# Kernel tuning notes

Measured on AMD Instinct MI355X. Metric: run time of the kernel, lower is better.

## Reference

```python
import jax, jax.numpy as jnp
import numpy as np

B, V, K = 4, 16384, 16
E, F, D, H, L, ITERS = 32, 2, 64, 4, 2, 10
NEG = -1e9


def setup_inputs() -> dict:
    key = jax.random.key(0)
    ks = jax.random.split(key, 24)
    def g(k, shape, fan_in):
        return jax.random.normal(k, shape, dtype=jnp.float32) * (fan_in ** -0.5)
    inp = {}
    inp["node_embeddings"] = jax.random.normal(ks[0], (B, V, E), dtype=jnp.float32)
    inp["node_features"] = jax.random.normal(ks[1], (B, V, F), dtype=jnp.float32)
    inp["demands"] = jax.random.normal(ks[2], (B, V, 1), dtype=jnp.float32)
    # padded adjacency list; value == V means masked (no neighbor)
    inp["adj_lst"] = jax.random.randint(ks[3], (B, V, K), 0, V + 1, dtype=jnp.int32)
    # precomputed inverse-adjacency indices; reference computes inflow by scatter-add instead
    inp["flow_indices"] = jax.random.randint(ks[4], (B, V, K), 0, V, dtype=jnp.int32)
    inp["num_nodes"] = V
    din = E + F
    inp["W_enc1"] = g(ks[5], (din, D), din); inp["b_enc1"] = jnp.zeros((D,), jnp.float32)
    inp["W_enc2"] = g(ks[6], (D, D), D); inp["b_enc2"] = jnp.zeros((D,), jnp.float32)
    inp["W_gat"] = g(ks[7], (H, D, D), D)
    inp["a_src"] = g(ks[8], (H, D), D)
    inp["a_dst"] = g(ks[9], (H, D), D)
    for i, nm in enumerate(["z", "r", "c"]):
        inp["W_" + nm] = g(ks[10 + 2 * i], (D, D), D)
        inp["U_" + nm] = g(ks[11 + 2 * i], (D, D), D)
        inp["b_" + nm] = jnp.zeros((D,), jnp.float32)
    inp["W_dec1"] = g(ks[16], (D, D), D); inp["b_dec1"] = jnp.zeros((D,), jnp.float32)
    inp["W_dec2"] = g(ks[17], (D, 1), D); inp["b_dec2"] = jnp.zeros((1,), jnp.float32)
    return inp


def _forward(node_embeddings, node_features, demands,
             W_enc1, b_enc1, W_enc2, b_enc2,
             W_gat, a_src, a_dst,
             W_z, U_z, b_z, W_r, U_r, b_r, W_c, U_c, b_c,
             W_dec1, b_dec1, W_dec2, b_dec2,
             adj_lst, num_nodes):
    Vn = num_nodes
    bidx = jnp.arange(adj_lst.shape[0])[:, None, None]  # [B,1,1]
    mask = adj_lst == Vn  # [B,V,K] padded slots

    # --- node encoder MLP (tanh, activate_final=True) ---
    x = jnp.concatenate([node_embeddings, node_features], axis=-1)
    h = jnp.tanh(x @ W_enc1 + b_enc1)
    h = jnp.tanh(h @ W_enc2 + b_enc2)

    def gather_nodes(t):
        # masked_gather: pad with a zero row so index == num_nodes reads zeros
        t_pad = jnp.concatenate([t, jnp.zeros_like(t[:, :1])], axis=1)  # [B,V+1,Dt]
        return t_pad[bidx, adj_lst]  # [B,V,K,Dt]

    # --- graph_layers x (AdjGAT + GRU) ---
    for _ in range(L):
        agg = 0.0
        for hd in range(H):
            t = h @ W_gat[hd]                       # [B,V,D]
            nb = gather_nodes(t)                    # [B,V,K,D]
            scores = (t @ a_src[hd])[:, :, None] + nb @ a_dst[hd]  # [B,V,K]
            attn = jax.nn.softmax(jnp.where(mask, NEG, scores), axis=-1)
            agg = agg + jnp.einsum('bvk,bvkd->bvd', attn, nb)
        m = jnp.tanh(agg / H)
        z = jax.nn.sigmoid(m @ W_z + h @ U_z + b_z)
        r = jax.nn.sigmoid(m @ W_r + h @ U_r + b_r)
        c = jnp.tanh(m @ W_c + (r * h) @ U_c + b_c)
        h = (1.0 - z) * h + z * c

    # --- decoder -> per-edge weights via masked gather + softmax ---
    node_w = jnp.tanh(h @ W_dec1 + b_dec1) @ W_dec2 + b_dec2   # [B,V,1]
    pw = gather_nodes(node_w)[..., 0]                          # [B,V,K]
    norm_w = jax.nn.softmax(jnp.where(mask, NEG, pw), axis=-1)

    # --- iterative min-cost-flow solver ---
    flow0 = norm_w * jax.nn.relu(-demands)  # sources (demand<0) push supply
    def body(carry, _):
        flow, _ = carry
        inflow = jnp.zeros((flow.shape[0], Vn + 1), flow.dtype)
        inflow = inflow.at[bidx, adj_lst].add(flow)[:, :Vn]    # [B,V]
        new = norm_w * jax.nn.relu(inflow[..., None] - demands)
        return (new, flow), None
    (flow, pflow), _ = jax.lax.scan(body, (flow0, flow0), None, length=ITERS)

    flow_cost = jnp.sum(flow * flow, axis=(1, 2))  # quadratic cost_fn
    return flow, flow_cost, norm_w, pflow


def reference(node_embeddings, node_features, demands, adj_lst, flow_indices, num_nodes,
              W_enc1, b_enc1, W_enc2, b_enc2, W_gat, a_src, a_dst,
              W_z, U_z, b_z, W_r, U_r, b_r, W_c, U_c, b_c,
              W_dec1, b_dec1, W_dec2, b_dec2):
    # flow_indices is the precomputed inverse adjacency; inflow is computed
    # equivalently here by scatter-add over adj_lst.
    return _forward(node_embeddings, node_features, demands,
                    W_enc1, b_enc1, W_enc2, b_enc2,
                    W_gat, a_src, a_dst,
                    W_z, U_z, b_z, W_r, U_r, b_r, W_c, U_c, b_c,
                    W_dec1, b_dec1, W_dec2, b_dec2,
                    adj_lst, num_nodes)
```

## Files before the change

### kernel.cpp

```cpp
#include <hip/hip_runtime.h>
#include <stdint.h>
#include <math.h>

#define BN 4
#define VN 16384
#define KN 16
#define HN 4
#define NN (BN*VN)
#define EN (VN*KN)
#define CAP 64
#define NEGC (-1.0e9f)

typedef __attribute__((ext_vector_type(8))) short short8;
typedef __attribute__((ext_vector_type(4))) float floatx4;
typedef __attribute__((ext_vector_type(2))) float floatx2;
typedef unsigned short u16;
typedef unsigned int u32;

#define OFF_H      0ull
#define OFF_T      16777216ull
#define OFF_M      50331648ull
#define OFF_SSRC   67108864ull
#define OFF_SDST   68157440ull
#define OFF_NW     69206016ull
#define OFF_NV     69468160ull
#define OFF_CNT    69992448ull
#define OFF_PG     70254848ull
#define OFF_PZR    (OFF_PG  + 32768ull)
#define OFF_PC     (OFF_PZR + 32768ull)
#define OFF_PE1    (OFF_PC  + 16384ull)
#define OFF_PE2    (OFF_PE1 + 8192ull)
#define OFF_PD1    (OFF_PE2 + 8192ull)

__device__ __forceinline__ u16 f2bf(float x){
  union { float f; unsigned int u; } c; c.f = x;
  unsigned int r = c.u + 0x7fffu + ((c.u >> 16) & 1u);
  return (u16)(r >> 16);
}
__device__ __forceinline__ float bf2f(u16 s){
  union { unsigned int u; float f; } c; c.u = ((unsigned int)s) << 16;
  return c.f;
}
__device__ __forceinline__ float sigm(float x){ return 1.0f/(1.0f+expf(-x)); }

union S8 { short8 v; u16 u[8]; };
union FU { float f; u32 u; };

__global__ __launch_bounds__(256) void k_zero(u32* __restrict__ cnt)
{
  cnt[blockIdx.x*256 + threadIdx.x] = 0u;
}

__global__ __launch_bounds__(256) void k_pack(
    const float* __restrict__ Wg,  const float* __restrict__ Wz, const float* __restrict__ Uz,
    const float* __restrict__ Wr,  const float* __restrict__ Ur, const float* __restrict__ Wc,
    const float* __restrict__ Uc,  const float* __restrict__ We1, const float* __restrict__ We2,
    const float* __restrict__ Wd1,
    u16* __restrict__ pg, u16* __restrict__ pzr, u16* __restrict__ pc,
    u16* __restrict__ pe1, u16* __restrict__ pe2, u16* __restrict__ pd1)
{
  int e = blockIdx.x*256 + threadIdx.x;
  int el; u16* dst; int CN; int region;
  if      (e < 16384){ el = e;        dst = pg;  CN = 2; region = 0; }
  else if (e < 32768){ el = e-16384;  dst = pzr; CN = 4; region = 1; }
  else if (e < 40960){ el = e-32768;  dst = pc;  CN = 4; region = 2; }
  else if (e < 45056){ el = e-40960;  dst = pe1; CN = 2; region = 3; }
  else if (e < 49152){ el = e-45056;  dst = pe2; CN = 2; region = 4; }
  else               { el = e-49152;  dst = pd1; CN = 2; region = 5; }
  int j    = el & 7;
  int lane = (el >> 3) & 63;
  int rest = el >> 9;
  int c  = rest % CN;
  int ng = rest / CN;
  int k  = c*32 + (lane>>4)*8 + j;
  int n  = ng*16 + (lane&15);
  float val = 0.0f;
  if (region == 0){
    val = Wg[(size_t)(n>>6)*4096 + k*64 + (n&63)];
  } else if (region == 1){
    int km = (k&3)*16 + ((k>>2)&15);
    if (n < 64) val = (k<64) ? Wz[km*64+n]      : Uz[(k-64)*64+n];
    else        val = (k<64) ? Wr[km*64+(n-64)] : Ur[(k-64)*64+(n-64)];
  } else if (region == 2){
    int km = (k&3)*16 + ((k>>2)&15);
    val = (k<64) ? Wc[km*64+n] : Uc[(k-64)*64+n];
  } else if (region == 3){
    val = (k<34) ? We1[k*64+n] : 0.0f;
  } else if (region == 4){
    val = We2[k*64+n];
  } else {
    val = Wd1[k*64+n];
  }
  dst[el] = f2bf(val);
}

template<int CN>
__device__ __forceinline__ void load_b(const u16* p, int chunk, int lane, short8 Bf[CN][4]){
  const short8* P = (const short8*)p;
  #pragma unroll
  for (int c=0;c<CN;c++)
    #pragma unroll
    for (int ng=0; ng<4; ng++)
      Bf[c][ng] = P[((chunk*4+ng)*CN + c)*64 + lane];
}

template<int CN>
__device__ __forceinline__ void mfma_tile(const short8* A, const short8 Bf[CN][4],
                                          floatx4 acc[4][4], int wave, int lane){
  #pragma unroll
  for (int c=0;c<CN;c++){
    #pragma unroll
    for (int mg=0;mg<4;mg++){
      short8 a = A[((wave*4+mg)*CN + c)*64 + lane];
      #pragma unroll
      for (int ng=0;ng<4;ng++)
        acc[mg][ng] = __builtin_amdgcn_mfma_f32_16x16x32_bf16(a, Bf[c][ng], acc[mg][ng], 0, 0, 0);
    }
  }
}

__device__ __forceinline__ void zero_acc(floatx4 acc[4][4]){
  #pragma unroll
  for (int mg=0;mg<4;mg++)
    #pragma unroll
    for (int ng=0;ng<4;ng++){
      floatx4 z = {0.f,0.f,0.f,0.f};
      acc[mg][ng] = z;
    }
}

__global__ __launch_bounds__(128) void k_enc(
    const float* __restrict__ emb, const float* __restrict__ feat,
    const u16* __restrict__ pe1, const u16* __restrict__ pe2,
    const float* __restrict__ be1, const float* __restrict__ be2,
    float* __restrict__ hout)
{
  __shared__ short8 A1[1024];
  __shared__ short8 A2[1024];
  const int tid = threadIdx.x;
  const int n0  = blockIdx.x * 128;
  for (int it=0; it<8; ++it){
    int slot = it*128 + tid;
    int row = slot >> 3, jc = slot & 7;
    S8 w;
    if (jc < 4){
      const float* s = emb + (size_t)(n0+row)*32 + jc*8;
      #pragma unroll
      for (int j=0;j<8;j++) w.u[j] = f2bf(s[j]);
    } else if (jc == 4){
      const float* s = feat + (size_t)(n0+row)*2;
      w.u[0] = f2bf(s[0]); w.u[1] = f2bf(s[1]);
      #pragma unroll
      for (int j=2;j<8;j++) w.u[j] = 0;
    } else {
      #pragma unroll
      for (int j=0;j<8;j++) w.u[j] = 0;
    }
    A1[((row>>4)*2 + (jc>>2))*64 + (jc&3)*16 + (row&15)] = w.v;
  }
  __syncthreads();
  const int wave = tid>>6, lane = tid&63, q = lane>>4, ml = lane&15;

  short8 Bf[2][4];
  load_b<2>(pe1, 0, lane, Bf);
  floatx4 acc[4][4];
  zero_acc(acc);
  mfma_tile<2>(A1, Bf, acc, wave, lane);

  u16* A2s = (u16*)A2;
  #pragma unroll
  for (int mg=0;mg<4;mg++){
    #pragma unroll
    for (int r=0;r<4;r++){
      int row_l = wave*64 + mg*16 + q*4 + r;
      #pragma unroll
      for (int ng=0;ng<4;ng++){
        int k2 = ng*16 + ml;
        float v = tanhf(acc[mg][ng][r] + be1[k2]);
        int c2 = k2>>5, q2=(k2>>3)&3, j2=k2&7;
        A2s[ (((row_l>>4)*2 + c2)*64 + q2*16 + (row_l&15))*8 + j2 ] = f2bf(v);
      }
    }
  }
  __syncthreads();

  load_b<2>(pe2, 0, lane, Bf);
  zero_acc(acc);
  mfma_tile<2>(A2, Bf, acc, wave, lane);
  #pragma unroll
  for (int mg=0;mg<4;mg++)
    #pragma unroll
    for (int r=0;r<4;r++){
      int row = n0 + wave*64 + mg*16 + q*4 + r;
      #pragma unroll
      for (int ng=0;ng<4;ng++){
        int col = ng*16 + ml;
        hout[(size_t)row*64 + col] = tanhf(acc[mg][ng][r] + be2[col]);
      }
    }
}

__global__ __launch_bounds__(128) void k_t(
    const float* __restrict__ h, const u16* __restrict__ pg,
    const float* __restrict__ asrc, const float* __restrict__ adst,
    u32* __restrict__ tq, float* __restrict__ ssrc, float* __restrict__ sdst)
{
  __shared__ short8 A[1024];
  const int tid = threadIdx.x;
  const int n0  = blockIdx.x * 128;
  for (int it=0; it<8; ++it){
    int slot = it*128 + tid;
    int row = slot >> 3, jc = slot & 7;
    const float* s = h + (size_t)(n0+row)*64 + jc*8;
    S8 w;
    #pragma unroll
    for (int j=0;j<8;j++) w.u[j] = f2bf(s[j]);
    A[((row>>4)*2 + (jc>>2))*64 + (jc&3)*16 + (row&15)] = w.v;
  }
  __syncthreads();
  const int wave = tid>>6, lane = tid&63, q = lane>>4, ml = lane&15;

  for (int chunk=0; chunk<4; ++chunk){
    short8 Bf[2][4];
    load_b<2>(pg, chunk, lane, Bf);
    floatx4 acc[4][4];
    zero_acc(acc);
    mfma_tile<2>(A, Bf, acc, wave, lane);

    float as[4], ad[4];
    #pragma unroll
    for (int ng=0;ng<4;ng++){
      as[ng] = asrc[chunk*64 + ng*16 + ml];
      ad[ng] = adst[chunk*64 + ng*16 + ml];
    }
    #pragma unroll
    for (int mg=0;mg<4;mg++){
      #pragma unroll
      for (int r=0;r<4;r++){
        int row = n0 + wave*64 + mg*16 + q*4 + r;
        float v0 = acc[mg][0][r], v1 = acc[mg][1][r];
        float v2 = acc[mg][2][r], v3 = acc[mg][3][r];
        int pk = __builtin_amdgcn_cvt_pk_fp8_f32(v0, v1, 0, false);
        pk     = __builtin_amdgcn_cvt_pk_fp8_f32(v2, v3, pk, true);
        tq[(size_t)row*64 + chunk*16 + ml] = (u32)pk;
        float ps = v0*as[0] + v1*as[1] + v2*as[2] + v3*as[3];
        float pd = v0*ad[0] + v1*ad[1] + v2*ad[2] + v3*ad[3];
        #pragma unroll
        for (int s=1;s<16;s<<=1){ ps += __shfl_xor(ps, s, 64); pd += __shfl_xor(pd, s, 64); }
        if (ml == 0){ ssrc[row*4 + chunk] = ps; sdst[row*4 + chunk] = pd; }
      }
    }
  }
}

__global__ __launch_bounds__(256) void k_attn(
    const int* __restrict__ adj, const u32* __restrict__ tq,
    const float* __restrict__ ssrc, const float* __restrict__ sdst,
    float* __restrict__ m)
{
  const int wave = threadIdx.x>>6, lane = threadIdx.x&63;
  const int nid = blockIdx.x*4 + wave;
  const int b = nid >> 14;
  const int hd = lane>>4;
  int u = adj[(size_t)nid*16 + (lane&15)];
  float sc = (u == VN) ? NEGC : (ssrc[nid*4 + hd] + sdst[((size_t)b*VN + u)*4 + hd]);
  float mx = sc;
  #pragma unroll
  for (int s=1;s<16;s<<=1) mx = fmaxf(mx, __shfl_xor(mx, s, 64));
  float ex = expf(sc - mx);
  float sm = ex;
  #pragma unroll
  for (int s=1;s<16;s<<=1) sm += __shfl_xor(sm, s, 64);
  float attn = ex / sm;

  float a0=0.f, a1=0.f, a2=0.f, a3=0.f;
  const int srcl = lane & 48;
  #pragma unroll
  for (int k2=0;k2<16;k2++){
    int u2 = __shfl(u, k2, 64);
    float av = __shfl(attn, srcl + k2, 64);
    u32 w = tq[((size_t)b*VN + u2)*64 + lane];
    floatx2 f01 = __builtin_amdgcn_cvt_pk_f32_fp8((int)w, false);
    floatx2 f23 = __builtin_amdgcn_cvt_pk_f32_fp8((int)w, true);
    a0 += av*f01.x; a1 += av*f01.y; a2 += av*f23.x; a3 += av*f23.y;
  }
  a0 += __shfl_xor(a0,16,64); a0 += __shfl_xor(a0,32,64);
  a1 += __shfl_xor(a1,16,64); a1 += __shfl_xor(a1,32,64);
  a2 += __shfl_xor(a2,16,64); a2 += __shfl_xor(a2,32,64);
  a3 += __shfl_xor(a3,16,64); a3 += __shfl_xor(a3,32,64);
  if (lane < 16){
    floatx4 val;
    val[0] = tanhf(a0*0.25f); val[1] = tanhf(a1*0.25f);
    val[2] = tanhf(a2*0.25f); val[3] = tanhf(a3*0.25f);
    *(floatx4*)(m + (size_t)nid*64 + lane*4) = val;
  }
}

__global__ __launch_bounds__(128) void k_gru(
    const float* __restrict__ m, float* __restrict__ h,
    const u16* __restrict__ pzr, const u16* __restrict__ pc_,
    const float* __restrict__ bz, const float* __restrict__ br,
    const float* __restrict__ bc_)
{
  __shared__ short8 A[2048];
  const int tid = threadIdx.x;
  const int n0  = blockIdx.x * 128;
  for (int it=0; it<16; ++it){
    int slot = it*128 + tid;
    int row = slot >> 4, jc = slot & 15;
    const float* s = (jc < 8) ? (m + (size_t)(n0+row)*64 + jc*8)
                              : (h + (size_t)(n0+row)*64 + (jc-8)*8);
    S8 w;
    #pragma unroll
    for (int j=0;j<8;j++) w.u[j] = f2bf(s[j]);
    A[((row>>4)*4 + (jc>>2))*64 + (jc&3)*16 + (row&15)] = w.v;
  }
  __syncthreads();
  const int wave = tid>>6, lane = tid&63, q = lane>>4, ml = lane&15;

  short8 Bf[4][4];

  floatx4 zacc[4][4];
  load_b<4>(pzr, 0, lane, Bf);
  zero_acc(zacc);
  mfma_tile<4>(A, Bf, zacc, wave, lane);

  floatx4 acc[4][4];
  load_b<4>(pzr, 1, lane, Bf);
  zero_acc(acc);
  mfma_tile<4>(A, Bf, acc, wave, lane);

  floatx4 h_old[4][4];
  u16* As = (u16*)A;
  #pragma unroll
  for (int mg=0;mg<4;mg++){
    #pragma unroll
    for (int r=0;r<4;r++){
      int row_l = wave*64 + mg*16 + q*4 + r;
      int row   = n0 + row_l;
      #pragma unroll
      for (int ng=0;ng<4;ng++){
        int col = ng*16 + ml;
        float rv = sigm(acc[mg][ng][r] + br[col]);
        float hv = h[(size_t)row*64 + col];
        h_old[mg][ng][r] = hv;
        int kk = 64 + col;
        int c2 = kk>>5, q2 = (kk>>3)&3, j2 = kk&7;
        As[ (((row_l>>4)*4 + c2)*64 + q2*16 + (row_l&15))*8 + j2 ] = f2bf(hv*rv);
      }
    }
  }

  load_b<4>(pc_, 0, lane, Bf);
  zero_acc(acc);
  mfma_tile<4>(A, Bf, acc, wave, lane);

  #pragma unroll
  for (int mg=0;mg<4;mg++)
    #pragma unroll
    for (int r=0;r<4;r++){
      int row = n0 + wave*64 + mg*16 + q*4 + r;
      #pragma unroll
      for (int ng=0;ng<4;ng++){
        int col = ng*16 + ml;
        float zv = sigm(zacc[mg][ng][r] + bz[col]);
        float cv = tanhf(acc[mg][ng][r] + bc_[col]);
        float ho = h_old[mg][ng][r];
        h[(size_t)row*64 + col] = (1.f - zv)*ho + zv*cv;
      }
    }
}

__global__ __launch_bounds__(128) void k_dec(
    const float* __restrict__ h, const u16* __restrict__ pd1,
    const float* __restrict__ bd1, const float* __restrict__ Wd2, const float* __restrict__ bd2,
    float* __restrict__ nodew, float* __restrict__ cost)
{
  {
    int t = blockIdx.x*128 + threadIdx.x;
    if (t < BN) cost[t] = 0.f;
  }
  __shared__ short8 A[1024];
  const int tid = threadIdx.x;
  const int n0  = blockIdx.x * 128;
  for (int it=0; it<8; ++it){
    int slot = it*128 + tid;
    int row = slot >> 3, jc = slot & 7;
    const float* s = h + (size_t)(n0+row)*64 + jc*8;
    S8 w;
    #pragma unroll
    for (int j=0;j<8;j++) w.u[j] = f2bf(s[j]);
    A[((row>>4)*2 + (jc>>2))*64 + (jc&3)*16 + (row&15)] = w.v;
  }
  __syncthreads();
  const int wave = tid>>6, lane = tid&63, q = lane>>4, ml = lane&15;

  short8 Bf[2][4];
  load_b<2>(pd1, 0, lane, Bf);
  floatx4 acc[4][4];
  zero_acc(acc);
  mfma_tile<2>(A, Bf, acc, wave, lane);

  float wd2l[4];
  #pragma unroll
  for (int ng=0;ng<4;ng++) wd2l[ng] = Wd2[ng*16 + ml];
  float b2 = bd2[0];
  #pragma unroll
  for (int mg=0;mg<4;mg++)
    #pragma unroll
    for (int r=0;r<4;r++){
      int row = n0 + wave*64 + mg*16 + q*4 + r;
      float ps = 0.f;
      #pragma unroll
      for (int ng=0;ng<4;ng++)
        ps += tanhf(acc[mg][ng][r] + bd1[ng*16+ml]) * wd2l[ng];
      #pragma unroll
      for (int s=1;s<16;s<<=1) ps += __shfl_xor(ps, s, 64);
      if (ml == 0) nodew[row] = ps + b2;
    }
}

__global__ __launch_bounds__(256) void k_pw(
    const int* __restrict__ adj, const float* __restrict__ nodew, const float* __restrict__ dem,
    float* __restrict__ normw, float* __restrict__ nv0,
    u32* __restrict__ cnt, uint2* __restrict__ bucket)
{
  int e = blockIdx.x*256 + threadIdx.x;
  int node = e >> 4;
  int b = node >> 14;
  int u = adj[e];
  float pw = (u == VN) ? NEGC : nodew[(size_t)b*VN + u];
  float mx = pw;
  #pragma unroll
  for (int s=1;s<16;s<<=1) mx = fmaxf(mx, __shfl_xor(mx, s, 64));
  float ex = expf(pw - mx);
  float sm = ex;
  #pragma unroll
  for (int s=1;s<16;s<<=1) sm += __shfl_xor(sm, s, 64);
  float nw = ex / sm;
  normw[e] = nw;
  if ((e & 15) == 0) nv0[node] = fmaxf(-dem[node], 0.f);
  if (u < VN){
    int g = b*VN + u;
    u32 pos = atomicAdd(&cnt[g], 1u);
    if (pos < CAP){
      FU fu; fu.f = nw;
      uint2 rec; rec.x = fu.u; rec.y = (u32)(node & (VN-1));
      bucket[(size_t)g*CAP + pos] = rec;
    }
  }
}

__global__ __launch_bounds__(256) void k_gather(
    const u32* __restrict__ cnt, const uint2* __restrict__ bucket,
    const float* __restrict__ dem, const float* __restrict__ nvin, float* __restrict__ nvout)
{
  int tid = blockIdx.x*256 + threadIdx.x;
  int g = tid >> 4;
  int lane = tid & 15;
  int b = g >> 14;
  u32 n = cnt[g];
  if (n > CAP) n = CAP;
  const uint2* bk = bucket + (size_t)g*CAP;
  const float* nb = nvin + (size_t)b*VN;
  float sum = 0.f;
  for (u32 i = (u32)lane; i < n; i += 16u){
    uint2 r = bk[i];
    FU fu; fu.u = r.x;
    sum += fu.f * nb[r.y];
  }
  #pragma unroll
  for (int sh=1; sh<16; sh<<=1) sum += __shfl_xor(sum, sh, 64);
  if (lane == 0) nvout[g] = fmaxf(sum - dem[g], 0.f);
}

__global__ __launch_bounds__(256) void k_flows(
    const float* __restrict__ normw, const float* __restrict__ nv9,
    const float* __restrict__ nv10,
    float* __restrict__ pflow, float* __restrict__ flow, float* __restrict__ cost)
{
  int e = blockIdx.x*256 + threadIdx.x;
  int node = e >> 4;
  float w = normw[e];
  pflow[e] = w * nv9[node];
  float fl = w * nv10[node];
  flow[e] = fl;
  float ss = fl*fl;
  #pragma unroll
  for (int sh=1; sh<64; sh<<=1) ss += __shfl_xor(ss, sh, 64);
  __shared__ float part[4];
  if ((threadIdx.x & 63) == 0) part[threadIdx.x>>6] = ss;
  __syncthreads();
  if (threadIdx.x == 0) atomicAdd(cost + (e>>18), part[0]+part[1]+part[2]+part[3]);
}

extern "C" void kernel_launch(void* const* d_in, const int* in_sizes, int n_in,
                              void* d_out, int out_size, void* d_ws, size_t ws_size,
                              hipStream_t stream)
{
  const float* emb  = (const float*)d_in[0];
  const float* feat = (const float*)d_in[1];
  const float* dem  = (const float*)d_in[2];
  const int*   adj  = (const int*)  d_in[3];
  const float* We1 = (const float*)d_in[6];
  const float* be1 = (const float*)d_in[7];
  const float* We2 = (const float*)d_in[8];
  const float* be2 = (const float*)d_in[9];
  const float* Wg  = (const float*)d_in[10];
  const float* asrc= (const float*)d_in[11];
  const float* adst= (const float*)d_in[12];
  const float* Wz  = (const float*)d_in[13];
  const float* Uz  = (const float*)d_in[14];
  const float* bz  = (const float*)d_in[15];
  const float* Wr  = (const float*)d_in[16];
  const float* Ur  = (const float*)d_in[17];
  const float* br  = (const float*)d_in[18];
  const float* Wc  = (const float*)d_in[19];
  const float* Uc  = (const float*)d_in[20];
  const float* bc  = (const float*)d_in[21];
  const float* Wd1 = (const float*)d_in[22];
  const float* bd1 = (const float*)d_in[23];
  const float* Wd2 = (const float*)d_in[24];
  const float* bd2 = (const float*)d_in[25];

  char* ws = (char*)d_ws;
  float* h     = (float*)(ws + OFF_H);
  u32*   tq    = (u32*)  (ws + OFF_T);
  uint2* bucket= (uint2*)(ws + OFF_T);
  float* m     = (float*)(ws + OFF_M);
  float* ssrc  = (float*)(ws + OFF_SSRC);
  float* sdst  = (float*)(ws + OFF_SDST);
  float* nodew = (float*)(ws + OFF_NW);
  float* nv    = (float*)(ws + OFF_NV);
  u32*   cnt   = (u32*)  (ws + OFF_CNT);
  u16* pg  = (u16*)(ws + OFF_PG);
  u16* pzr = (u16*)(ws + OFF_PZR);
  u16* pc  = (u16*)(ws + OFF_PC);
  u16* pe1 = (u16*)(ws + OFF_PE1);
  u16* pe2 = (u16*)(ws + OFF_PE2);
  u16* pd1 = (u16*)(ws + OFF_PD1);
  float* nv0b = nv;
  float* nv1b = nv + NN;

  float* out0 = (float*)d_out;
  float* out1 = out0 + 1048576;
  float* out2 = out0 + 1048580;
  float* out3 = out0 + 2097156;

  k_zero<<<256, 256, 0, stream>>>(cnt);
  k_pack<<<208, 256, 0, stream>>>(Wg, Wz, Uz, Wr, Ur, Wc, Uc, We1, We2, Wd1,
                                  pg, pzr, pc, pe1, pe2, pd1);
  k_enc<<<512, 128, 0, stream>>>(emb, feat, pe1, pe2, be1, be2, h);

  for (int l=0; l<2; ++l){
    k_t   <<<512, 128, 0, stream>>>(h, pg, asrc, adst, tq, ssrc, sdst);
    k_attn<<<16384, 256, 0, stream>>>(adj, tq, ssrc, sdst, m);
    k_gru <<<512, 128, 0, stream>>>(m, h, pzr, pc, bz, br, bc);
  }

  k_dec<<<512, 128, 0, stream>>>(h, pd1, bd1, Wd2, bd2, nodew, out1);
  k_pw <<<4096, 256, 0, stream>>>(adj, nodew, dem, out2, nv0b, cnt, bucket);

  for (int i=1; i<=10; ++i){
    float* in  = (i & 1) ? nv0b : nv1b;
    float* out = (i & 1) ? nv1b : nv0b;
    k_gather<<<4096, 256, 0, stream>>>(cnt, bucket, dem, in, out);
  }
  k_flows<<<4096, 256, 0, stream>>>(out2, nv1b, nv0b, out3, out0, out1);
}
```

Measured before the change: 500.4 us.

## Store hidden state, messages and flow buckets in bf16; fold counter zeroing into encoder

Hidden state h and message tensor m are now stored as bf16 instead of fp32, so k_t, k_gru and k_dec load packed short8 rows straight into LDS without converting. Flow bucket records shrink from 8 to 4 bytes by packing a bf16 weight with a 16-bit node index. The separate counter-zeroing kernel is merged into k_enc, saving one launch. The aim is less memory traffic in the layer and gather loops, at the cost of extra rounding in the GRU recurrence state and in the edge weights used by the flow iterations.

Measured after the change: 481.3 us. 1.04x faster.

```diff
diff --git a/kernel.cpp b/kernel.cpp
--- a/kernel.cpp
+++ b/kernel.cpp
@@ -18,14 +18,14 @@
 typedef unsigned int u32;
 
 #define OFF_H      0ull
+#define OFF_M      8388608ull
 #define OFF_T      16777216ull
-#define OFF_M      50331648ull
-#define OFF_SSRC   67108864ull
-#define OFF_SDST   68157440ull
-#define OFF_NW     69206016ull
-#define OFF_NV     69468160ull
-#define OFF_CNT    69992448ull
-#define OFF_PG     70254848ull
+#define OFF_SSRC   50331648ull
+#define OFF_SDST   51380224ull
+#define OFF_NW     52428800ull
+#define OFF_NV     52690944ull
+#define OFF_CNT    53215232ull
+#define OFF_PG     53477376ull
 #define OFF_PZR    (OFF_PG  + 32768ull)
 #define OFF_PC     (OFF_PZR + 32768ull)
 #define OFF_PE1    (OFF_PC  + 16384ull)
@@ -37,19 +37,13 @@
   unsigned int r = c.u + 0x7fffu + ((c.u >> 16) & 1u);
   return (u16)(r >> 16);
 }
-__device__ __forceinline__ float bf2f(u16 s){
-  union { unsigned int u; float f; } c; c.u = ((unsigned int)s) << 16;
+__device__ __forceinline__ float bf2f(u32 s){
+  union { unsigned int u; float f; } c; c.u = s << 16;
   return c.f;
 }
 __device__ __forceinline__ float sigm(float x){ return 1.0f/(1.0f+expf(-x)); }
 
 union S8 { short8 v; u16 u[8]; };
-union FU { float f; u32 u; };
-
-__global__ __launch_bounds__(256) void k_zero(u32* __restrict__ cnt)
-{
-  cnt[blockIdx.x*256 + threadIdx.x] = 0u;
-}
 
 __global__ __launch_bounds__(256) void k_pack(
     const float* __restrict__ Wg,  const float* __restrict__ Wz, const float* __restrict__ Uz,
@@ -133,8 +127,9 @@
     const float* __restrict__ emb, const float* __restrict__ feat,
     const u16* __restrict__ pe1, const u16* __restrict__ pe2,
     const float* __restrict__ be1, const float* __restrict__ be2,
-    float* __restrict__ hout)
-{
+    u16* __restrict__ hout, u32* __restrict__ cnt)
+{
+  cnt[blockIdx.x*128 + threadIdx.x] = 0u;
   __shared__ short8 A1[1024];
   __shared__ short8 A2[1024];
   const int tid = threadIdx.x;
@@ -195,27 +190,24 @@
       #pragma unroll
       for (int ng=0;ng<4;ng++){
         int col = ng*16 + ml;
-        hout[(size_t)row*64 + col] = tanhf(acc[mg][ng][r] + be2[col]);
+        hout[(size_t)row*64 + col] = f2bf(tanhf(acc[mg][ng][r] + be2[col]));
       }
     }
 }
 
 __global__ __launch_bounds__(128) void k_t(
-    const float* __restrict__ h, const u16* __restrict__ pg,
+    const u16* __restrict__ h, const u16* __restrict__ pg,
     const float* __restrict__ asrc, const float* __restrict__ adst,
     u32* __restrict__ tq, float* __restrict__ ssrc, float* __restrict__ sdst)
 {
   __shared__ short8 A[1024];
   const int tid = threadIdx.x;
   const int n0  = blockIdx.x * 128;
+  const short8* hp = (const short8*)h;
   for (int it=0; it<8; ++it){
     int slot = it*128 + tid;
     int row = slot >> 3, jc = slot & 7;
-    const float* s = h + (size_t)(n0+row)*64 + jc*8;
-    S8 w;
-    #pragma unroll
-    for (int j=0;j<8;j++) w.u[j] = f2bf(s[j]);
-    A[((row>>4)*2 + (jc>>2))*64 + (jc&3)*16 + (row&15)] = w.v;
+    A[((row>>4)*2 + (jc>>2))*64 + (jc&3)*16 + (row&15)] = hp[(size_t)(n0+row)*8 + jc];
   }
   __syncthreads();
   const int wave = tid>>6, lane = tid&63, q = lane>>4, ml = lane&15;
@@ -256,7 +248,7 @@
 __global__ __launch_bounds__(256) void k_attn(
     const int* __restrict__ adj, const u32* __restrict__ tq,
     const float* __restrict__ ssrc, const float* __restrict__ sdst,
-    float* __restrict__ m)
+    u16* __restrict__ m)
 {
   const int wave = threadIdx.x>>6, lane = threadIdx.x&63;
   const int nid = blockIdx.x*4 + wave;
@@ -289,15 +281,15 @@
   a2 += __shfl_xor(a2,16,64); a2 += __shfl_xor(a2,32,64);
   a3 += __shfl_xor(a3,16,64); a3 += __shfl_xor(a3,32,64);
   if (lane < 16){
-    floatx4 val;
-    val[0] = tanhf(a0*0.25f); val[1] = tanhf(a1*0.25f);
-    val[2] = tanhf(a2*0.25f); val[3] = tanhf(a3*0.25f);
-    *(floatx4*)(m + (size_t)nid*64 + lane*4) = val;
+    union { uint2 v; u16 u[4]; } val;
+    val.u[0] = f2bf(tanhf(a0*0.25f)); val.u[1] = f2bf(tanhf(a1*0.25f));
+    val.u[2] = f2bf(tanhf(a2*0.25f)); val.u[3] = f2bf(tanhf(a3*0.25f));
+    *(uint2*)(m + (size_t)nid*64 + lane*4) = val.v;
   }
 }
 
 __global__ __launch_bounds__(128) void k_gru(
-    const float* __restrict__ m, float* __restrict__ h,
+    const u16* __restrict__ m, u16* __restrict__ h,
     const u16* __restrict__ pzr, const u16* __restrict__ pc_,
     const float* __restrict__ bz, const float* __restrict__ br,
     const float* __restrict__ bc_)
@@ -305,15 +297,14 @@
   __shared__ short8 A[2048];
   const int tid = threadIdx.x;
   const int n0  = blockIdx.x * 128;
+  const short8* mp = (const short8*)m;
+  const short8* hp = (const short8*)h;
   for (int it=0; it<16; ++it){
     int slot = it*128 + tid;
     int row = slot >> 4, jc = slot & 15;
-    const float* s = (jc < 8) ? (m + (size_t)(n0+row)*64 + jc*8)
-                              : (h + (size_t)(n0+row)*64 + (jc-8)*8);
-    S8 w;
-    #pragma unroll
-    for (int j=0;j<8;j++) w.u[j] = f2bf(s[j]);
-    A[((row>>4)*4 + (jc>>2))*64 + (jc&3)*16 + (row&15)] = w.v;
+    short8 w = (jc < 8) ? mp[(size_t)(n0+row)*8 + jc]
+                        : hp[(size_t)(n0+row)*8 + (jc-8)];
+    A[((row>>4)*4 + (jc>>2))*64 + (jc&3)*16 + (row&15)] = w;
   }
   __syncthreads();
   const int wave = tid>>6, lane = tid&63, q = lane>>4, ml = lane&15;
@@ -342,7 +333,7 @@
       for (int ng=0;ng<4;ng++){
         int col = ng*16 + ml;
         float rv = sigm(acc[mg][ng][r] + br[col]);
-        float hv = h[(size_t)row*64 + col];
+        float hv = bf2f(h[(size_t)row*64 + col]);
         h_old[mg][ng][r] = hv;
         int kk = 64 + col;
         int c2 = kk>>5, q2 = (kk>>3)&3, j2 = kk&7;
@@ -366,13 +357,13 @@
         float zv = sigm(zacc[mg][ng][r] + bz[col]);
         float cv = tanhf(acc[mg][ng][r] + bc_[col]);
         float ho = h_old[mg][ng][r];
-        h[(size_t)row*64 + col] = (1.f - zv)*ho + zv*cv;
+        h[(size_t)row*64 + col] = f2bf((1.f - zv)*ho + zv*cv);
       }
     }
 }
 
 __global__ __launch_bounds__(128) void k_dec(
-    const float* __restrict__ h, const u16* __restrict__ pd1,
+    const u16* __restrict__ h, const u16* __restrict__ pd1,
     const float* __restrict__ bd1, const float* __restrict__ Wd2, const float* __restrict__ bd2,
     float* __restrict__ nodew, float* __restrict__ cost)
 {
@@ -383,14 +374,11 @@
   __shared__ short8 A[1024];
   const int tid = threadIdx.x;
   const int n0  = blockIdx.x * 128;
+  const short8* hp = (const short8*)h;
   for (int it=0; it<8; ++it){
     int slot = it*128 + tid;
     int row = slot >> 3, jc = slot & 7;
-    const float* s = h + (size_t)(n0+row)*64 + jc*8;
-    S8 w;
-    #pragma unroll
-    for (int j=0;j<8;j++) w.u[j] = f2bf(s[j]);
-    A[((row>>4)*2 + (jc>>2))*64 + (jc&3)*16 + (row&15)] = w.v;
+    A[((row>>4)*2 + (jc>>2))*64 + (jc&3)*16 + (row&15)] = hp[(size_t)(n0+row)*8 + jc];
   }
   __syncthreads();
   const int wave = tid>>6, lane = tid&63, q = lane>>4, ml = lane&15;
@@ -423,7 +411,7 @@
 __global__ __launch_bounds__(256) void k_pw(
     const int* __restrict__ adj, const float* __restrict__ nodew, const float* __restrict__ dem,
     float* __restrict__ normw, float* __restrict__ nv0,
-    u32* __restrict__ cnt, uint2* __restrict__ bucket)
+    u32* __restrict__ cnt, u32* __restrict__ bucket)
 {
   int e = blockIdx.x*256 + threadIdx.x;
   int node = e >> 4;
@@ -443,16 +431,13 @@
   if (u < VN){
     int g = b*VN + u;
     u32 pos = atomicAdd(&cnt[g], 1u);
-    if (pos < CAP){
-      FU fu; fu.f = nw;
-      uint2 rec; rec.x = fu.u; rec.y = (u32)(node & (VN-1));
-      bucket[(size_t)g*CAP + pos] = rec;
-    }
+    if (pos < CAP)
+      bucket[(size_t)g*CAP + pos] = ((u32)f2bf(nw) << 16) | (u32)(node & (VN-1));
   }
 }
 
 __global__ __launch_bounds__(256) void k_gather(
-    const u32* __restrict__ cnt, const uint2* __restrict__ bucket,
+    const u32* __restrict__ cnt, const u32* __restrict__ bucket,
     const float* __restrict__ dem, const float* __restrict__ nvin, float* __restrict__ nvout)
 {
   int tid = blockIdx.x*256 + threadIdx.x;
@@ -461,13 +446,12 @@
   int b = g >> 14;
   u32 n = cnt[g];
   if (n > CAP) n = CAP;
-  const uint2* bk = bucket + (size_t)g*CAP;
+  const u32* bk = bucket + (size_t)g*CAP;
   const float* nb = nvin + (size_t)b*VN;
   float sum = 0.f;
   for (u32 i = (u32)lane; i < n; i += 16u){
-    uint2 r = bk[i];
-    FU fu; fu.u = r.x;
-    sum += fu.f * nb[r.y];
+    u32 r = bk[i];
+    sum += bf2f(r >> 16) * nb[r & 0xFFFFu];
   }
   #pragma unroll
   for (int sh=1; sh<16; sh<<=1) sum += __shfl_xor(sum, sh, 64);
@@ -524,10 +508,10 @@
   const float* bd2 = (const float*)d_in[25];
 
   char* ws = (char*)d_ws;
-  float* h     = (float*)(ws + OFF_H);
+  u16*   h     = (u16*)  (ws + OFF_H);
+  u16*   m     = (u16*)  (ws + OFF_M);
   u32*   tq    = (u32*)  (ws + OFF_T);
-  uint2* bucket= (uint2*)(ws + OFF_T);
-  float* m     = (float*)(ws + OFF_M);
+  u32*   bucket= (u32*)  (ws + OFF_T);
   float* ssrc  = (float*)(ws + OFF_SSRC);
   float* sdst  = (float*)(ws + OFF_SDST);
   float* nodew = (float*)(ws + OFF_NW);
@@ -547,10 +531,9 @@
   float* out2 = out0 + 1048580;
   float* out3 = out0 + 2097156;
 
-  k_zero<<<256, 256, 0, stream>>>(cnt);
   k_pack<<<208, 256, 0, stream>>>(Wg, Wz, Uz, Wr, Ur, Wc, Uc, We1, We2, Wd1,
                                   pg, pzr, pc, pe1, pe2, pd1);
-  k_enc<<<512, 128, 0, stream>>>(emb, feat, pe1, pe2, be1, be2, h);
+  k_enc<<<512, 128, 0, stream>>>(emb, feat, pe1, pe2, be1, be2, h, cnt);
 
   for (int l=0; l<2; ++l){
     k_t   <<<512, 128, 0, stream>>>(h, pg, asrc, adst, tq, ssrc, sdst);
```
